# Optimization experiments

Measured on AMD Instinct MI355X. Metric: run time of the kernel, lower is better.

Reference implementation:

```python
import jax, jax.numpy as jnp
import numpy as np

P, N, F, H, O = 64, 256, 4096, 512, 64  # pathways, genes/pathway, cells, hidden, output

def setup_inputs() -> dict:
    key = jax.random.key(0)
    k = jax.random.split(key, 6)
    s = lambda fan_in: 1.0 / np.sqrt(fan_in)
    return {
        "lpls": jax.random.normal(k[0], (P, N, N), jnp.float32),
        "exp":  jax.random.normal(k[1], (P, N, F), jnp.float32),
        "W1":   jax.random.normal(k[2], (P, N, H), jnp.float32) * s(N),
        "b1":   jax.random.normal(k[3], (P, H), jnp.float32) * s(N),
        "W2":   jax.random.normal(k[4], (P, H, O), jnp.float32) * s(H),
        "b2":   jax.random.normal(k[5], (P, O), jnp.float32) * s(H),
    }

def reference(lpls, exp, W1, b1, W2, b2):
    # Grouped Laplacian aggregation: c_exp[p] = lpls[p] @ exp[p]  -> [P, N, F]
    c = jnp.einsum('pnm,pmf->pnf', lpls, exp)
    # Transpose: MLP runs over cells, features = genes-in-pathway -> [P, F, N]
    x = jnp.swapaxes(c, 1, 2)
    h = jax.nn.relu(jnp.einsum('pfn,pnh->pfh', x, W1) + b1[:, None, :])
    out = jnp.einsum('pfh,pho->pfo', h, W2) + b2[:, None, :]
    return out  # [P, F, O]; row p corresponds to output_cal_l[p]
```

## Files before the change

### kernel.cpp

```cpp
#include <hip/hip_runtime.h>
#include <hip/hip_bf16.h>
#include <stdint.h>

#define P_ 64
#define N_ 256
#define F_ 4096
#define H_ 512
#define O_ 64

#define FT 128
#define HC 128
#define KC 64

using fragA = __attribute__((ext_vector_type(8))) short;
using fragC = __attribute__((ext_vector_type(4))) float;

__device__ __forceinline__ short f2bf(float f) {
    union { float f; unsigned u; } v; v.f = f;
    unsigned r = v.u + 0x7fffu + ((v.u >> 16) & 1u);
    return (short)(r >> 16);
}

__device__ __forceinline__ void gload_lds16(const void* g, void* l) {
    __builtin_amdgcn_global_load_lds(
        (const __attribute__((address_space(1))) unsigned*)g,
        (__attribute__((address_space(3))) unsigned*)l,
        16, 0, 0);
}

__device__ __forceinline__ int hswz(int frow) {
    return (((frow >> 2) & 3) ^ (frow & 3)) << 4;
}

__global__ __launch_bounds__(256) void k_transpose_cvt(
    const float* __restrict__ in, short* __restrict__ out, int R, int C)
{
    __shared__ float t[32][33];
    int b = blockIdx.z;
    int tx = threadIdx.x & 31, ty = threadIdx.x >> 5;
    int r0 = blockIdx.y * 32, c0 = blockIdx.x * 32;
    const float* ip = in + ((size_t)b * R + r0) * C + c0;
    #pragma unroll
    for (int i = 0; i < 4; ++i)
        t[ty + 8*i][tx] = ip[(size_t)(ty + 8*i) * C + tx];
    __syncthreads();
    short* op = out + ((size_t)b * C + c0) * R + r0;
    #pragma unroll
    for (int i = 0; i < 4; ++i)
        op[(size_t)(ty + 8*i) * R + tx] = f2bf(t[tx][ty + 8*i]);
}

__global__ __launch_bounds__(256) void k_fold(
    const short* __restrict__ w1T,
    const short* __restrict__ lplsT,
    short* __restrict__ w1t)
{
    int tid = threadIdx.x;
    int w = tid >> 6, l = tid & 63, lg = l >> 4, lr = l & 15;
    int bp = blockIdx.x;
    int p  = bp >> 3;
    int hb = ((bp >> 1) & 3) * 128;
    int nb = (bp & 1) * 128;
    int wr = w >> 1, wc = w & 1;

    const short* A = w1T   + (size_t)p * H_ * 256;
    const short* B = lplsT + (size_t)p * N_ * 256;

    fragC acc[4][4];
    #pragma unroll
    for (int i = 0; i < 4; ++i)
        #pragma unroll
        for (int j = 0; j < 4; ++j)
            acc[i][j] = fragC{0.f, 0.f, 0.f, 0.f};

    #pragma unroll
    for (int kk = 0; kk < 8; ++kk) {
        fragA af[4], bf[4];
        #pragma unroll
        for (int mi = 0; mi < 4; ++mi) {
            int h = hb + wr*64 + mi*16 + lr;
            af[mi] = *(const fragA*)&A[(size_t)h*256 + kk*32 + lg*8];
        }
        #pragma unroll
        for (int nj = 0; nj < 4; ++nj) {
            int n = nb + wc*64 + nj*16 + lr;
            bf[nj] = *(const fragA*)&B[(size_t)n*256 + kk*32 + lg*8];
        }
        #pragma unroll
        for (int mi = 0; mi < 4; ++mi)
            #pragma unroll
            for (int nj = 0; nj < 4; ++nj)
                acc[mi][nj] = __builtin_amdgcn_mfma_f32_16x16x32_bf16(
                    af[mi], bf[nj], acc[mi][nj], 0, 0, 0);
    }

    #pragma unroll
    for (int mi = 0; mi < 4; ++mi)
        #pragma unroll
        for (int nj = 0; nj < 4; ++nj)
            #pragma unroll
            for (int r = 0; r < 4; ++r) {
                int h = hb + wr*64 + mi*16 + lg*4 + r;
                int n = nb + wc*64 + nj*16 + lr;
                w1t[((size_t)(p*H_ + h)) * N_ + n] = f2bf(acc[mi][nj][r]);
            }
}

__global__ __launch_bounds__(512) void k_mlp(
    const float* __restrict__ expm,
    const short* __restrict__ w1t,
    const float* __restrict__ b1,
    const short* __restrict__ w2t,
    const float* __restrict__ b2,
    float* __restrict__ out)
{
    __shared__ __align__(16) short hlds[FT][HC];
    __shared__ __align__(16) short wbuf[2][HC][KC];

    int tid = threadIdx.x;
    int w = tid >> 6, l = tid & 63, lg = l >> 4, lr = l & 15;
    int p  = blockIdx.x >> 5;
    int f0 = (blockIdx.x & 31) * FT;
    int fw = f0 + w*16 + lr;

    auto STAGE = [&](int s) {
        int hcs = s >> 2, kcs = s & 3;
        #pragma unroll
        for (int i = 0; i < 2; ++i) {
            int lin = i*512 + tid;
            int hl  = lin >> 3;
            int s8  = (lin & 7) * 8;
            int nsg = s8 ^ ((hl & 7) << 3);
            const short* src = w1t + ((size_t)(p*H_ + hcs*HC + hl)) * N_ + kcs*KC + nsg;
            short* dst = &wbuf[s & 1][0][0] + i*4096 + w*512;
            gload_lds16(src, dst);
        }
    };

    fragA a[8];
    const float* eb = expm + (size_t)p * N_ * F_ + fw;
    #pragma unroll
    for (int kk = 0; kk < 8; ++kk) {
        #pragma unroll
        for (int e = 0; e < 8; ++e) {
            int n = kk*32 + lg*8 + e;
            a[kk][e] = f2bf(eb[(size_t)n * F_]);
        }
    }

    fragC oacc[4];
    #pragma unroll
    for (int q = 0; q < 4; ++q) oacc[q] = fragC{0.f, 0.f, 0.f, 0.f};

    STAGE(0);

    #pragma unroll 1
    for (int hc = 0; hc < 4; ++hc) {
        int hb0 = hc * HC;

        fragC acc2[8];
        #pragma unroll
        for (int q = 0; q < 8; ++q) acc2[q] = fragC{0.f, 0.f, 0.f, 0.f};

        #pragma unroll
        for (int kc = 0; kc < 4; ++kc) {
            int s = hc*4 + kc;
            asm volatile("s_waitcnt vmcnt(0)" ::: "memory");
            __syncthreads();
            if (s + 1 < 16) STAGE(s + 1);

            #pragma unroll
            for (int kh = 0; kh < 2; ++kh) {
                #pragma unroll
                for (int q = 0; q < 8; ++q) {
                    int hl = q*16 + lr;
                    int ns = (kh*32 + lg*8) ^ ((hl & 7) << 3);
                    fragA b = *(const fragA*)&wbuf[s & 1][hl][ns];
                    acc2[q] = __builtin_amdgcn_mfma_f32_16x16x32_bf16(
                        a[kc*2 + kh], b, acc2[q], 0, 0, 0);
                }
            }
        }

        #pragma unroll
        for (int q = 0; q < 8; ++q) {
            int hcol = q*16 + lr;
            float bv = b1[p*H_ + hb0 + hcol];
            #pragma unroll
            for (int r = 0; r < 4; ++r) {
                int frow = w*16 + lg*4 + r;
                float v = acc2[q][r] + bv;
                v = fmaxf(v, 0.f);
                hlds[frow][hcol ^ hswz(frow)] = f2bf(v);
            }
        }

        #pragma unroll
        for (int k3 = 0; k3 < 4; ++k3) {
            int frow = w*16 + lr;
            int hloc = k3*32 + lg*8;
            fragA a3 = *(const fragA*)&hlds[frow][hloc ^ hswz(frow)];
            #pragma unroll
            for (int q3 = 0; q3 < 4; ++q3) {
                const short* wsrc = w2t + ((size_t)(p*O_ + q3*16 + lr)) * H_
                                        + hb0 + k3*32 + lg*8;
                fragA b3 = *(const fragA*)wsrc;
                oacc[q3] = __builtin_amdgcn_mfma_f32_16x16x32_bf16(
                    a3, b3, oacc[q3], 0, 0, 0);
            }
        }
    }

    #pragma unroll
    for (int q3 = 0; q3 < 4; ++q3) {
        int o = q3*16 + lr;
        float bv = b2[p*O_ + o];
        #pragma unroll
        for (int r = 0; r < 4; ++r) {
            int f = f0 + w*16 + lg*4 + r;
            out[((size_t)(p*F_ + f)) * O_ + o] = oacc[q3][r] + bv;
        }
    }
}

extern "C" void kernel_launch(void* const* d_in, const int* in_sizes, int n_in,
                              void* d_out, int out_size, void* d_ws, size_t ws_size,
                              hipStream_t stream) {
    const float* lpls = (const float*)d_in[0];
    const float* expm = (const float*)d_in[1];
    const float* W1   = (const float*)d_in[2];
    const float* b1   = (const float*)d_in[3];
    const float* W2   = (const float*)d_in[4];
    const float* b2   = (const float*)d_in[5];
    float* outp = (float*)d_out;

    char* base = (char*)d_ws;
    short* lplsT = (short*)(base);
    short* w1T   = (short*)(base + 8388608);
    short* w1t   = (short*)(base + 8388608 + 16777216);
    short* w2t   = (short*)(base + 8388608 + 2*16777216);

    k_transpose_cvt<<<dim3(N_/32, N_/32, P_), 256, 0, stream>>>(lpls, lplsT, N_, N_);
    k_transpose_cvt<<<dim3(H_/32, N_/32, P_), 256, 0, stream>>>(W1,   w1T,   N_, H_);
    k_transpose_cvt<<<dim3(O_/32, H_/32, P_), 256, 0, stream>>>(W2,   w2t,   H_, O_);
    k_fold<<<512, 256, 0, stream>>>(w1T, lplsT, w1t);
    k_mlp<<<P_ * (F_ / FT), 512, 0, stream>>>(expm, w1t, b1, w2t, b2, outp);
}
```

Before: 660.6 us.

## Triple-buffer W1 staging, vectorize transposes, remap blocks, overlap exp loads

The MLP kernel moves from a double-buffered to a triple-buffered LDS ring for the folded W1 tiles. It waits with vmcnt(2) so one stage stays in flight, and it issues two stages before the loop. The exp loads are split into two halves so the first stages are issued between them, and block indices are remapped so that consecutive blocks spread across pathways. The transpose kernels now use 64x64 tiles with float4 loads and ushort4 stores, and launch_bounds adds an occupancy hint. The extra LDS buffer and the register staging arrays can lower occupancy.

```diff
diff --git a/kernel.cpp b/kernel.cpp
--- a/kernel.cpp
+++ b/kernel.cpp
@@ -35,19 +35,31 @@
 __global__ __launch_bounds__(256) void k_transpose_cvt(
     const float* __restrict__ in, short* __restrict__ out, int R, int C)
 {
-    __shared__ float t[32][33];
+    __shared__ float t[64][65];
     int b = blockIdx.z;
-    int tx = threadIdx.x & 31, ty = threadIdx.x >> 5;
-    int r0 = blockIdx.y * 32, c0 = blockIdx.x * 32;
+    int r0 = blockIdx.y * 64, c0 = blockIdx.x * 64;
+    int tid = threadIdx.x;
     const float* ip = in + ((size_t)b * R + r0) * C + c0;
     #pragma unroll
-    for (int i = 0; i < 4; ++i)
-        t[ty + 8*i][tx] = ip[(size_t)(ty + 8*i) * C + tx];
+    for (int it = 0; it < 4; ++it) {
+        int flat = it*256 + tid;
+        int r = flat >> 4, cq = (flat & 15) * 4;
+        float4 v = *(const float4*)&ip[(size_t)r * C + cq];
+        t[r][cq+0] = v.x; t[r][cq+1] = v.y; t[r][cq+2] = v.z; t[r][cq+3] = v.w;
+    }
     __syncthreads();
     short* op = out + ((size_t)b * C + c0) * R + r0;
     #pragma unroll
-    for (int i = 0; i < 4; ++i)
-        op[(size_t)(ty + 8*i) * R + tx] = f2bf(t[tx][ty + 8*i]);
+    for (int it = 0; it < 4; ++it) {
+        int flat = it*256 + tid;
+        int c = flat >> 4, rq = (flat & 15) * 4;
+        ushort4 v;
+        v.x = (unsigned short)f2bf(t[rq+0][c]);
+        v.y = (unsigned short)f2bf(t[rq+1][c]);
+        v.z = (unsigned short)f2bf(t[rq+2][c]);
+        v.w = (unsigned short)f2bf(t[rq+3][c]);
+        *(ushort4*)&op[(size_t)c * R + rq] = v;
+    }
 }
 
 __global__ __launch_bounds__(256) void k_fold(
@@ -106,7 +118,7 @@
             }
 }
 
-__global__ __launch_bounds__(512) void k_mlp(
+__global__ __launch_bounds__(512, 4) void k_mlp(
     const float* __restrict__ expm,
     const short* __restrict__ w1t,
     const float* __restrict__ b1,
@@ -115,16 +127,18 @@
     float* __restrict__ out)
 {
     __shared__ __align__(16) short hlds[FT][HC];
-    __shared__ __align__(16) short wbuf[2][HC][KC];
+    __shared__ __align__(16) short wbuf[3][HC*KC];
 
     int tid = threadIdx.x;
     int w = tid >> 6, l = tid & 63, lg = l >> 4, lr = l & 15;
-    int p  = blockIdx.x >> 5;
-    int f0 = (blockIdx.x & 31) * FT;
+    int bid = (int)blockIdx.x;
+    int b2v = (bid & 7) * 256 + (bid >> 3);
+    int p  = b2v >> 5;
+    int f0 = (b2v & 31) * FT;
     int fw = f0 + w*16 + lr;
 
     auto STAGE = [&](int s) {
-        int hcs = s >> 2, kcs = s & 3;
+        int hcs = s >> 2, kcs = s & 3, bsel = s % 3;
         #pragma unroll
         for (int i = 0; i < 2; ++i) {
             int lin = i*512 + tid;
@@ -132,27 +146,40 @@
             int s8  = (lin & 7) * 8;
             int nsg = s8 ^ ((hl & 7) << 3);
             const short* src = w1t + ((size_t)(p*H_ + hcs*HC + hl)) * N_ + kcs*KC + nsg;
-            short* dst = &wbuf[s & 1][0][0] + i*4096 + w*512;
+            short* dst = &wbuf[0][0] + bsel*8192 + i*4096 + w*512;
             gload_lds16(src, dst);
         }
     };
 
+    const float* eb = expm + (size_t)p * N_ * F_ + fw;
+    float raw0[32], raw1[32];
+    #pragma unroll
+    for (int kk = 0; kk < 4; ++kk)
+        #pragma unroll
+        for (int e = 0; e < 8; ++e)
+            raw0[kk*8+e] = eb[(size_t)(kk*32 + lg*8 + e) * F_];
+    STAGE(0); STAGE(1);
+    #pragma unroll
+    for (int kk = 0; kk < 4; ++kk)
+        #pragma unroll
+        for (int e = 0; e < 8; ++e)
+            raw1[kk*8+e] = eb[(size_t)((kk+4)*32 + lg*8 + e) * F_];
+
     fragA a[8];
-    const float* eb = expm + (size_t)p * N_ * F_ + fw;
-    #pragma unroll
-    for (int kk = 0; kk < 8; ++kk) {
-        #pragma unroll
-        for (int e = 0; e < 8; ++e) {
-            int n = kk*32 + lg*8 + e;
-            a[kk][e] = f2bf(eb[(size_t)n * F_]);
-        }
-    }
+    #pragma unroll
+    for (int kk = 0; kk < 4; ++kk)
+        #pragma unroll
+        for (int e = 0; e < 8; ++e)
+            a[kk][e] = f2bf(raw0[kk*8+e]);
+    #pragma unroll
+    for (int kk = 0; kk < 4; ++kk)
+        #pragma unroll
+        for (int e = 0; e < 8; ++e)
+            a[kk+4][e] = f2bf(raw1[kk*8+e]);
 
     fragC oacc[4];
     #pragma unroll
     for (int q = 0; q < 4; ++q) oacc[q] = fragC{0.f, 0.f, 0.f, 0.f};
-
-    STAGE(0);
 
     #pragma unroll 1
     for (int hc = 0; hc < 4; ++hc) {
@@ -165,17 +192,20 @@
         #pragma unroll
         for (int kc = 0; kc < 4; ++kc) {
             int s = hc*4 + kc;
-            asm volatile("s_waitcnt vmcnt(0)" ::: "memory");
-            __syncthreads();
-            if (s + 1 < 16) STAGE(s + 1);
-
+            if (hc == 3 && kc == 3) asm volatile("s_waitcnt vmcnt(0)" ::: "memory");
+            else                    asm volatile("s_waitcnt vmcnt(2)" ::: "memory");
+            __builtin_amdgcn_s_barrier();
+            __builtin_amdgcn_sched_barrier(0);
+            if (hc < 3 || kc < 2) STAGE(s + 2);
+
+            const short* wb = &wbuf[0][0] + (s % 3) * 8192;
             #pragma unroll
             for (int kh = 0; kh < 2; ++kh) {
                 #pragma unroll
                 for (int q = 0; q < 8; ++q) {
                     int hl = q*16 + lr;
                     int ns = (kh*32 + lg*8) ^ ((hl & 7) << 3);
-                    fragA b = *(const fragA*)&wbuf[s & 1][hl][ns];
+                    fragA b = *(const fragA*)&wb[hl*64 + ns];
                     acc2[q] = __builtin_amdgcn_mfma_f32_16x16x32_bf16(
                         a[kc*2 + kh], b, acc2[q], 0, 0, 0);
                 }
@@ -240,9 +270,9 @@
     short* w1t   = (short*)(base + 8388608 + 16777216);
     short* w2t   = (short*)(base + 8388608 + 2*16777216);
 
-    k_transpose_cvt<<<dim3(N_/32, N_/32, P_), 256, 0, stream>>>(lpls, lplsT, N_, N_);
-    k_transpose_cvt<<<dim3(H_/32, N_/32, P_), 256, 0, stream>>>(W1,   w1T,   N_, H_);
-    k_transpose_cvt<<<dim3(O_/32, H_/32, P_), 256, 0, stream>>>(W2,   w2t,   H_, O_);
+    k_transpose_cvt<<<dim3(N_/64, N_/64, P_), 256, 0, stream>>>(lpls, lplsT, N_, N_);
+    k_transpose_cvt<<<dim3(H_/64, N_/64, P_), 256, 0, stream>>>(W1,   w1T,   N_, H_);
+    k_transpose_cvt<<<dim3(O_/64, H_/64, P_), 256, 0, stream>>>(W2,   w2t,   H_, O_);
     k_fold<<<512, 256, 0, stream>>>(w1T, lplsT, w1t);
     k_mlp<<<P_ * (F_ / FT), 512, 0, stream>>>(expm, w1t, b1, w2t, b2, outp);
 }
```

After: 776.1 us. +17.5%, slower.
